# Kernel optimization log

Measured on AMD Instinct MI355X. Metric: run time of the kernel, lower is better.

## Reference

```python
import jax, jax.numpy as jnp
import numpy as np

B, V = 128, 128000
NEG_INF = float('-inf')


def _apply_top_k(logits, top_ks):
    vocab = logits.shape[-1]
    valid_k = jnp.where(top_ks > 0, jnp.minimum(top_ks, vocab), vocab)  # [B]
    order = jnp.argsort(-logits, axis=-1)                 # descending sort indices [B,V]
    sorted_logits = jnp.take_along_axis(logits, order, axis=-1)
    ranks = jnp.arange(vocab)[None, :]                    # [1,V]
    keep = ranks < valid_k[:, None]
    masked_sorted = jnp.where(keep, sorted_logits, NEG_INF)
    rows = jnp.arange(logits.shape[0])[:, None]
    return jnp.zeros_like(logits).at[rows, order].set(masked_sorted)


def _apply_top_p(logits, top_ps):
    order = jnp.argsort(-logits, axis=-1)
    sorted_logits = jnp.take_along_axis(logits, order, axis=-1)
    sorted_probs = jax.nn.softmax(sorted_logits, axis=-1)
    cum = jnp.cumsum(sorted_probs, axis=-1)
    keep = cum < top_ps[:, None]
    keep = keep.at[:, 0].set(True)                        # always keep the top token
    masked_sorted = jnp.where(keep, sorted_logits, NEG_INF)
    rows = jnp.arange(logits.shape[0])[:, None]
    return jnp.zeros_like(logits).at[rows, order].set(masked_sorted)


def setup_inputs() -> dict:
    key = jax.random.key(0)
    k1, k2, k3, k4, k5 = jax.random.split(key, 5)
    logits = jax.random.normal(k1, (B, V), dtype=jnp.float32) * 4.0
    temperatures = jax.random.uniform(k2, (B,), dtype=jnp.float32) + 0.5  # [0.5, 1.5)
    top_ks = jax.random.randint(k3, (B,), 0, 100, dtype=jnp.int64)        # 0 -> disabled
    top_ps = jax.random.uniform(k4, (B,), dtype=jnp.float32)
    # uniform noise; reference converts to Exp(1) via -log(u)
    exp_noise_u = jax.random.uniform(k5, (B, V), dtype=jnp.float32, minval=1e-12, maxval=1.0)
    return {"logits": logits, "temperatures": temperatures, "top_ks": top_ks,
            "top_ps": top_ps, "exp_noise_u": exp_noise_u}


def reference(logits, temperatures, top_ks, top_ps, exp_noise_u):
    x = logits.astype(jnp.float32) / temperatures[:, None]
    x = _apply_top_k(x, top_ks)
    x = _apply_top_p(x, top_ps)
    probs = jax.nn.softmax(x, axis=-1)
    q = jnp.clip(-jnp.log(exp_noise_u), 1e-10)            # Exp(1) samples, clamped like torch
    sample_tokens = jnp.argmax(probs / q, axis=-1)
    return sample_tokens
```

## Files before the change

kernel.cpp:

```cpp
#include <hip/hip_runtime.h>
#include <math.h>

#define SA 8
#define SEG2 8
#define NB 4096
#define TAA 512
#define HS 256
#define TE 512
#define TBB 1024
#define SCT 256
#define CH (NB / SCT)
#define CAPSEG 512
#define GTOT (SA * CAPSEG)
#define MAXM1 16
#define GB1 16384
#define SUBC 512
#define EQC 64
#define FXS 1099511627776.0f
#define FXI (1.0f / 1099511627776.0f)

typedef unsigned u32;
typedef unsigned long long u64;

struct ScanSh {
  u32 axc[SCT]; float axe[SCT];
  u32 sufc[SCT]; float sufe[SCT];
  int cbin[SCT]; u32 cca[SCT]; float cea[SCT];
  int fbin[SCT]; u32 fca[SCT]; float fea[SCT];
};

__device__ __forceinline__ u32 f2key(float f) {
  u32 u = __float_as_uint(f);
  return u ^ ((u >> 31) ? 0xFFFFFFFFu : 0x80000000u);
}
__device__ __forceinline__ int is_mode0(int k, int V) {
  return (k >= 1 && k <= 256 && k < V);
}

__device__ int m1_slot(const int* topks, int row, int V, int tid, int* red) {
  if (tid < 128) {
    int c = 0;
    for (int r = tid; r < row; r += 128) c += !is_mode0(topks[r], V);
    red[tid] = c;
  }
  __syncthreads();
  for (int s = 64; s > 0; s >>= 1) {
    if (tid < s) red[tid] += red[tid + s];
    __syncthreads();
  }
  return red[0];
}

__device__ __forceinline__ float row_max(const float* maxpart, int row) {
  float mm = maxpart[row * SA];
  for (int j = 1; j < SA; ++j) mm = fmaxf(mm, maxpart[row * SA + j]);
  return mm;
}

__device__ void scan_level(const u32* cnt, const u64* e0, ScanSh* ax,
                           u32* sprefix, int* scnt_above, float* sexp_above,
                           float target, int tid) {
  if (tid < SCT) {
    u32 cc = 0; float ce = 0.f; const int base = tid * CH;
    for (int j = 0; j < CH; ++j) { cc += cnt[base + j]; ce += (float)e0[base + j] * FXI; }
    ax->axc[tid] = cc; ax->axe[tid] = ce;
  }
  __syncthreads();
  if (tid == 0) {
    u32 rc = 0; float re = 0.f;
    for (int c = SCT - 1; c >= 0; --c) {
      ax->sufc[c] = rc; ax->sufe[c] = re;
      rc += ax->axc[c]; re += ax->axe[c];
    }
  }
  __syncthreads();
  if (tid < SCT) {
    const int base = tid * CH;
    u32 rc = ax->sufc[tid]; float re = ax->sufe[tid];
    int best = -1; u32 bca = 0; float bea = 0.f;
    int fb = -1; u32 ffca = 0; float ffea = 0.f;
    for (int b = base + CH - 1; b >= base; --b) {
      u32 c = cnt[b]; float ebv = (float)e0[b] * FXI;
      bool cross = (c > 0) && ((re + ebv) >= target);
      if (cross && best < 0) { best = b; bca = rc; bea = re; }
      if (c > 0) { fb = b; ffca = rc; ffea = re; }
      rc += c; re += ebv;
    }
    ax->cbin[tid] = best; ax->cca[tid] = bca; ax->cea[tid] = bea;
    ax->fbin[tid] = fb; ax->fca[tid] = ffca; ax->fea[tid] = ffea;
  }
  __syncthreads();
  if (tid == 0) {
    int bsel = -1; u32 ca = 0; float ea = 0.f;
    for (int c = 0; c < SCT; ++c) {
      int b = ax->cbin[c];
      if (b > bsel) { bsel = b; ca = ax->cca[c]; ea = ax->cea[c]; }
    }
    if (bsel < 0) {
      for (int c = 0; c < SCT; ++c) {
        int b = ax->fbin[c];
        if (b >= 0 && (bsel < 0 || b < bsel)) { bsel = b; ca = ax->fca[c]; ea = ax->fea[c]; }
      }
    }
    if (bsel < 0) bsel = 0;
    *sprefix = (u32)bsel;
    *scnt_above = (int)ca;
    *sexp_above = ea;
  }
  __syncthreads();
}

__global__ __launch_bounds__(TAA) void kA(const float* __restrict__ logits,
                                          const float* __restrict__ temps,
                                          const int* __restrict__ topks,
                                          float* __restrict__ maxpart,
                                          u32* __restrict__ scnt,
                                          float* __restrict__ candv,
                                          int* __restrict__ candi, int V) {
  const int row = blockIdx.x, seg = blockIdx.y, tid = threadIdx.x;
  __shared__ u32 cnt[NB];
  __shared__ float sm[TAA];
  __shared__ u32 cs[HS];
  __shared__ int bb[HS];
  __shared__ int lcnt;
  __shared__ u32 sT;
  const int k = topks[row];
  const int m0 = is_mode0(k, V);
  const float t = temps[row];
  const float* lr = logits + (size_t)row * V;
  const float4* l4 = (const float4*)lr;
  const int n4 = V >> 2;
  const int q0 = (int)((long long)seg * n4 / SA);
  const int q1 = (int)((long long)(seg + 1) * n4 / SA);
  float mx = -INFINITY;
  if (m0) {
    for (int i = tid; i < NB; i += TAA) cnt[i] = 0;
    if (tid == 0) lcnt = 0;
    __syncthreads();
    for (int i = q0 + tid; i < q1; i += TAA) {
      float4 v = l4[i];
      float xs[4] = {v.x / t, v.y / t, v.z / t, v.w / t};
#pragma unroll
      for (int j = 0; j < 4; ++j) {
        mx = fmaxf(mx, xs[j]);
        atomicAdd(&cnt[f2key(xs[j]) >> 20], 1u);
      }
    }
    if (seg == SA - 1)
      for (int i = (n4 << 2) + tid; i < V; i += TAA) {
        float x = lr[i] / t;
        mx = fmaxf(mx, x);
        atomicAdd(&cnt[f2key(x) >> 20], 1u);
      }
  } else {
    for (int i = q0 + tid; i < q1; i += TAA) {
      float4 v = l4[i];
      mx = fmaxf(mx, fmaxf(fmaxf(v.x, v.y), fmaxf(v.z, v.w)) / t);
    }
    if (seg == SA - 1)
      for (int i = (n4 << 2) + tid; i < V; i += TAA) mx = fmaxf(mx, lr[i] / t);
  }
  sm[tid] = mx;
  __syncthreads();
  for (int s = TAA >> 1; s > 0; s >>= 1) {
    if (tid < s) sm[tid] = fmaxf(sm[tid], sm[tid + s]);
    __syncthreads();
  }
  if (tid == 0) maxpart[row * SA + seg] = sm[0];
  if (!m0) return;
  if (tid < HS) {
    u32 cc = 0; const int base = tid * (NB / HS);
    for (int j = 0; j < NB / HS; ++j) cc += cnt[base + j];
    cs[tid] = cc;
  }
  __syncthreads();
  if (tid == 0) {
    u32 rc = 0;
    for (int c = HS - 1; c >= 0; --c) { u32 tmp = cs[c]; cs[c] = rc; rc += tmp; }
  }
  __syncthreads();
  const int kk = (k > 256) ? 256 : k;
  if (tid < HS) {
    const int base = tid * (NB / HS);
    u32 rc = cs[tid]; int best = -1;
    for (int b = base + NB / HS - 1; b >= base; --b) {
      u32 c = cnt[b];
      if (c && best < 0 && (int)(rc + c) >= kk) best = b;
      rc += c;
    }
    bb[tid] = best;
  }
  __syncthreads();
  if (tid == 0) {
    int bsel = -1;
    for (int c = 0; c < HS; ++c) if (bb[c] > bsel) bsel = bb[c];
    if (bsel < 0) { for (int b = 0; b < NB; ++b) if (cnt[b]) { bsel = b; break; } }
    if (bsel < 0) bsel = 0;
    sT = ((u32)bsel) << 20;
  }
  __syncthreads();
  const u32 T = sT;
  const size_t cbase = ((size_t)row * SA + seg) * CAPSEG;
  for (int i = q0 + tid; i < q1; i += TAA) {
    float4 v = l4[i];
    float xs[4] = {v.x / t, v.y / t, v.z / t, v.w / t};
#pragma unroll
    for (int j = 0; j < 4; ++j) {
      if (f2key(xs[j]) >= T) {
        int s = atomicAdd(&lcnt, 1);
        if (s < CAPSEG) { candv[cbase + s] = xs[j]; candi[cbase + s] = i * 4 + j; }
      }
    }
  }
  if (seg == SA - 1)
    for (int i = (n4 << 2) + tid; i < V; i += TAA) {
      float x = lr[i] / t;
      if (f2key(x) >= T) {
        int s = atomicAdd(&lcnt, 1);
        if (s < CAPSEG) { candv[cbase + s] = x; candi[cbase + s] = i; }
      }
    }
  __syncthreads();
  if (tid == 0) { int n = lcnt; if (n > CAPSEG) n = CAPSEG; scnt[row * SA + seg] = (u32)n; }
}

__global__ __launch_bounds__(TE) void kE(const float* __restrict__ logits,
                                         const float* __restrict__ temps,
                                         const int* __restrict__ topks,
                                         const float* __restrict__ maxpart,
                                         float* __restrict__ Sparts,
                                         u32* __restrict__ m1c0,
                                         u64* __restrict__ m1e0, int V) {
  const int row = blockIdx.x, seg = blockIdx.y, tid = threadIdx.x;
  const int k = topks[row];
  if (is_mode0(k, V)) return;
  __shared__ int red[128];
  const int slot = m1_slot(topks, row, V, tid, red);
  if (slot >= MAXM1) return;
  __shared__ u32 c0[NB];
  __shared__ u64 e0[NB];
  __shared__ float ss[TE];
  for (int i = tid; i < NB; i += TE) { c0[i] = 0; e0[i] = 0ull; }
  __syncthreads();
  const float t = temps[row];
  const float m = row_max(maxpart, row);
  const float* lr = logits + (size_t)row * V;
  const float4* l4 = (const float4*)lr;
  const int n4 = V >> 2;
  const int q0 = (int)((long long)seg * n4 / SEG2);
  const int q1 = (int)((long long)(seg + 1) * n4 / SEG2);
  float ls = 0.f;
  for (int i = q0 + tid; i < q1; i += TE) {
    float4 v = l4[i];
    float xs[4] = {v.x / t, v.y / t, v.z / t, v.w / t};
#pragma unroll
    for (int j = 0; j < 4; ++j) {
      float e = expf(xs[j] - m);
      ls += e;
      u32 b = f2key(xs[j]) >> 20;
      atomicAdd(&c0[b], 1u);
      u64 fx = (u64)(e * FXS);
      if (fx) atomicAdd(&e0[b], fx);
    }
  }
  if (seg == SEG2 - 1)
    for (int i = (n4 << 2) + tid; i < V; i += TE) {
      float x = lr[i] / t;
      float e = expf(x - m);
      ls += e;
      u32 b = f2key(x) >> 20;
      atomicAdd(&c0[b], 1u);
      u64 fx = (u64)(e * FXS);
      if (fx) atomicAdd(&e0[b], fx);
    }
  ss[tid] = ls;
  __syncthreads();
  for (int s = TE >> 1; s > 0; s >>= 1) {
    if (tid < s) ss[tid] += ss[tid + s];
    __syncthreads();
  }
  if (tid == 0) Sparts[slot * SEG2 + seg] = ss[0];
  for (int b = tid; b < NB; b += TE) {
    u32 c = c0[b]; if (c) atomicAdd(&m1c0[(size_t)slot * NB + b], c);
    u64 e = e0[b]; if (e) atomicAdd(&m1e0[(size_t)slot * NB + b], e);
  }
}

__global__ __launch_bounds__(TBB) void kM1(const float* __restrict__ logits,
                                           const float* __restrict__ temps,
                                           const int* __restrict__ topks,
                                           const float* __restrict__ topps,
                                           const float* __restrict__ noise,
                                           const float* __restrict__ maxpart,
                                           const float* __restrict__ Sparts,
                                           const u32* __restrict__ m1c0,
                                           const u64* __restrict__ m1e0,
                                           u64* __restrict__ g1p,
                                           u32* __restrict__ gcnt,
                                           u64* __restrict__ rpack,
                                           u32* __restrict__ rdone,
                                           int* __restrict__ out, int V) {
  const int row = blockIdx.x, seg = blockIdx.y, tid = threadIdx.x;
  const int k = topks[row];
  if (is_mode0(k, V)) return;
  __shared__ int red[128];
  const int slot = m1_slot(topks, row, V, tid, red);
  if (slot >= MAXM1) return;

  __shared__ u32 cnt[NB];
  __shared__ u64 e0[NB];
  __shared__ ScanSh ax;
  __shared__ u32 spfx; __shared__ int sca; __shared__ float sea;
  __shared__ float rr[TBB]; __shared__ int ri[TBB];
  for (int i = tid; i < NB; i += TBB) {
    cnt[i] = m1c0[(size_t)slot * NB + i];
    e0[i] = m1e0[(size_t)slot * NB + i];
  }
  __syncthreads();
  float S = 0.f;
  for (int j = 0; j < SEG2; ++j) S += Sparts[slot * SEG2 + j];
  const float target = topps[row] * S;
  scan_level(cnt, e0, &ax, &spfx, &sca, &sea, target, tid);
  const u32 pfx = spfx;

  const float t = temps[row];
  const float m = row_max(maxpart, row);
  const float* lr = logits + (size_t)row * V;
  const float* ur = noise + (size_t)row * V;
  const float4* l4 = (const float4*)lr;
  const float4* u4 = (const float4*)ur;
  const int n4 = V >> 2;
  const int q0 = (int)((long long)seg * n4 / SEG2);
  const int q1 = (int)((long long)(seg + 1) * n4 / SEG2);
  const size_t gbase = (size_t)slot * GB1;

  float best = -1.f; int bidx = 0x7FFFFFFF;
  for (int i = q0 + tid; i < q1; i += TBB) {
    float4 xv = l4[i];
    float4 uv = u4[i];
    float xs[4] = {xv.x / t, xv.y / t, xv.z / t, xv.w / t};
    float us[4] = {uv.x, uv.y, uv.z, uv.w};
#pragma unroll
    for (int j = 0; j < 4; ++j) {
      u32 key = f2key(xs[j]);
      u32 bin = key >> 20;
      int idx = i * 4 + j;
      if (bin == pfx) {
        u32 s2 = atomicAdd(&gcnt[slot], 1u);
        if (s2 < GB1)
          atomicExch(&g1p[gbase + s2],
                     ((u64)__float_as_uint(xs[j]) << 32) | (u64)(u32)idx);
      } else if (bin > pfx) {
        float q = fmaxf(-logf(us[j]), 1e-10f);
        float rt = expf(xs[j] - m) / q;
        if (rt > best || (rt == best && idx < bidx)) { best = rt; bidx = idx; }
      }
    }
  }
  if (seg == SEG2 - 1)
    for (int i = (n4 << 2) + tid; i < V; i += TBB) {
      float x = lr[i] / t;
      u32 key = f2key(x);
      u32 bin = key >> 20;
      if (bin == pfx) {
        u32 s2 = atomicAdd(&gcnt[slot], 1u);
        if (s2 < GB1)
          atomicExch(&g1p[gbase + s2],
                     ((u64)__float_as_uint(x) << 32) | (u64)(u32)i);
      } else if (bin > pfx) {
        float q = fmaxf(-logf(ur[i]), 1e-10f);
        float rt = expf(x - m) / q;
        if (rt > best || (rt == best && i < bidx)) { best = rt; bidx = i; }
      }
    }
  rr[tid] = best; ri[tid] = bidx;
  __syncthreads();
  for (int s = TBB >> 1; s > 0; s >>= 1) {
    if (tid < s) {
      float ov = rr[tid + s]; int oi = ri[tid + s];
      if (ov > rr[tid] || (ov == rr[tid] && oi < ri[tid])) { rr[tid] = ov; ri[tid] = oi; }
    }
    __syncthreads();
  }
  __shared__ int slast;
  if (tid == 0) {
    if (rr[0] >= 0.f) {
      u64 pk = ((u64)f2key(rr[0]) << 32) | (u64)(0xFFFFFFFFu - (u32)ri[0]);
      atomicMax(&rpack[row], pk);
    }
    __threadfence();
    u32 arr = atomicAdd(&rdone[row], 1u);
    slast = (arr == (u32)(SEG2 - 1)) ? 1 : 0;
  }
  __syncthreads();
  if (!slast) return;
  __threadfence();

  __shared__ u32 cnt1[1024]; __shared__ u64 fx1[1024];
  __shared__ u32 csuf[1024]; __shared__ u64 esuf[1024];
  __shared__ float subv[SUBC]; __shared__ int subi[SUBC];
  __shared__ float ssv[SUBC]; __shared__ int ssi[SUBC];
  __shared__ int eqs[EQC];
  __shared__ int scross, sfb, sca1, sns, seqn;
  __shared__ float sea1; __shared__ u32 svstar;

  int nf = (int)atomicAdd(&gcnt[slot], 0u);
  if (nf > GB1) nf = GB1;
  cnt1[tid] = 0; fx1[tid] = 0ull;
  if (tid == 0) { sns = 0; scross = -1; sfb = 0x7FFFFFFF; }
  __syncthreads();
  for (int i = tid; i < nf; i += TBB) {
    u64 p = atomicAdd(&g1p[gbase + i], 0ull);
    float x = __uint_as_float((u32)(p >> 32));
    u32 b = (f2key(x) >> 10) & 0x3FFu;
    float e = expf(x - m);
    atomicAdd(&cnt1[b], 1u);
    u64 fx = (u64)(e * FXS);
    if (fx) atomicAdd(&fx1[b], fx);
  }
  __syncthreads();
  csuf[tid] = cnt1[tid]; esuf[tid] = fx1[tid];
  __syncthreads();
  for (int stp = 1; stp < 1024; stp <<= 1) {
    u32 ca_ = 0; u64 ea_ = 0ull;
    if (tid + stp < 1024) { ca_ = csuf[tid + stp]; ea_ = esuf[tid + stp]; }
    __syncthreads();
    csuf[tid] += ca_; esuf[tid] += ea_;
    __syncthreads();
  }
  {
    u32 c = cnt1[tid];
    if (c) {
      float racc = (float)(esuf[tid] - fx1[tid]) * FXI;
      float ebv = (float)fx1[tid] * FXI;
      if (sea + (racc + ebv) >= target) atomicMax(&scross, tid);
      atomicMin(&sfb, tid);
    }
  }
  __syncthreads();
  if (tid == 0) {
    int cb = scross;
    if (cb < 0) cb = (sfb != 0x7FFFFFFF) ? sfb : 0;
    u32 cAbove = csuf[cb] - cnt1[cb];
    float eAbove = (float)(esuf[cb] - fx1[cb]) * FXI;
    scross = cb;
    sea1 = sea + eAbove;
    sca1 = sca + (int)cAbove;
  }
  __syncthreads();
  const u32 cb = (u32)scross;
  for (int i = tid; i < nf; i += TBB) {
    u64 p = atomicAdd(&g1p[gbase + i], 0ull);
    float x = __uint_as_float((u32)(p >> 32));
    if (((f2key(x) >> 10) & 0x3FFu) == cb) {
      int s2 = atomicAdd(&sns, 1);
      if (s2 < SUBC) { subv[s2] = x; subi[s2] = (int)(u32)(p & 0xFFFFFFFFull); }
    }
  }
  __syncthreads();
  int ns = sns; if (ns > SUBC) ns = SUBC;
  for (int i = tid; i < ns; i += TBB) {
    float v = subv[i]; int ix = subi[i];
    int rank = 0;
    for (int j2 = 0; j2 < ns; ++j2) {
      float vj = subv[j2]; int ij = subi[j2];
      if (vj > v || (vj == v && ij < ix)) rank++;
    }
    ssv[rank] = v; ssi[rank] = ix;
  }
  __syncthreads();
  if (tid == 0) {
    const float p = topps[row];
    float run_n = sea1 / S;
    const int have_above = (sca1 > 0);
    u32 lastkey = 0u; int lastr = 0, laststart = -1, anykept = 0;
    u32 vsel = 0u; int rsel = -1, bstart = 0;
    int j = 0;
    while (j < ns) {
      u32 key = f2key(ssv[j]);
      int c = 1;
      while (j + c < ns && f2key(ssv[j + c]) == key) ++c;
      float e = expf(ssv[j] - m);
      float en = e / S;
      int kept = 0;
      for (int q = 0; q < c; ++q) {
        float nn = run_n + en;
        if (nn < p) { run_n = nn; kept++; } else break;
      }
      if (kept == c) { lastkey = key; lastr = c; laststart = j; anykept = 1; j += c; continue; }
      if (kept > 0) { vsel = key; rsel = kept; bstart = j; }
      else if (anykept) { vsel = lastkey; rsel = lastr; bstart = laststart; }
      else if (have_above) { vsel = key; rsel = 0; bstart = j; }
      else { vsel = key; rsel = 1; bstart = j; }
      break;
    }
    if (rsel < 0) {
      if (anykept) { vsel = lastkey; rsel = lastr; bstart = laststart; }
      else if (ns > 0) {
        vsel = f2key(ssv[0]); bstart = 0;
        rsel = have_above ? 0 : 1;
      } else { vsel = 0u; rsel = 0; bstart = 0; }
    }
    int eqn = rsel;
    if (eqn > EQC) eqn = EQC;
    if (eqn < 0) eqn = 0;
    if (bstart + eqn > ns) eqn = ns - bstart;
    if (eqn < 0) eqn = 0;
    for (int q2 = 0; q2 < eqn; ++q2) eqs[q2] = ssi[bstart + q2];
    seqn = eqn; svstar = vsel;
  }
  __syncthreads();

  const u32 vk = svstar;
  const int eqn = seqn;
  best = -1.f; bidx = 0x7FFFFFFF;
  for (int i = tid; i < nf; i += TBB) {
    u64 p = atomicAdd(&g1p[gbase + i], 0ull);
    float x = __uint_as_float((u32)(p >> 32));
    int ix = (int)(u32)(p & 0xFFFFFFFFull);
    u32 key = f2key(x);
    bool kept = key > vk;
    if (!kept && key == vk) {
      for (int e = 0; e < eqn; ++e) if (eqs[e] == ix) { kept = true; break; }
    }
    if (kept) {
      float q = fmaxf(-logf(ur[ix]), 1e-10f);
      float rt = expf(x - m) / q;
      if (rt > best || (rt == best && ix < bidx)) { best = rt; bidx = ix; }
    }
  }
  rr[tid] = best; ri[tid] = bidx;
  __syncthreads();
  for (int s = TBB >> 1; s > 0; s >>= 1) {
    if (tid < s) {
      float ov = rr[tid + s]; int oi = ri[tid + s];
      if (ov > rr[tid] || (ov == rr[tid] && oi < ri[tid])) { rr[tid] = ov; ri[tid] = oi; }
    }
    __syncthreads();
  }
  if (tid == 0) {
    u64 myPk = 0ull;
    if (rr[0] >= 0.f)
      myPk = ((u64)f2key(rr[0]) << 32) | (u64)(0xFFFFFFFFu - (u32)ri[0]);
    u64 prev = atomicMax(&rpack[row], myPk);
    u64 fin = prev > myPk ? prev : myPk;
    out[row] = (int)(0xFFFFFFFFu - (u32)(fin & 0xFFFFFFFFull));
  }
}

__global__ __launch_bounds__(TBB) void kH(const float* __restrict__ topps,
                                          const float* __restrict__ noise,
                                          const int* __restrict__ topks,
                                          const float* __restrict__ maxpart,
                                          const u32* __restrict__ scnt,
                                          const float* __restrict__ candv,
                                          const int* __restrict__ candi,
                                          int* __restrict__ out, int V) {
  const int row = blockIdx.x, tid = threadIdx.x;
  const int kR = topks[row];
  if (!is_mode0(kR, V)) return;
  __shared__ float gv[GTOT]; __shared__ int gi[GTOT];
  __shared__ float sv[CAPSEG]; __shared__ int si[CAPSEG];
  __shared__ float fv[CAPSEG]; __shared__ int fi[CAPSEG];
  __shared__ float pe[CAPSEG];
  __shared__ float rr[TBB]; __shared__ int ri[TBB];
  __shared__ int offs[SA + 1];
  __shared__ u32 dh[256]; __shared__ u32 dsufx[256];
  __shared__ u32 sPrefix; __shared__ int sRemain, sNf, sDig;
  __shared__ int sJ; __shared__ float sZ2;
  if (tid == 0) {
    int o = 0;
    for (int s = 0; s < SA; ++s) {
      offs[s] = o;
      int c = (int)scnt[row * SA + s];
      if (c > CAPSEG) c = CAPSEG;
      if (c < 0) c = 0;
      o += c;
    }
    offs[SA] = o;
  }
  __syncthreads();
  const int g = offs[SA];
  for (int s = 0; s < SA; ++s) {
    const int o = offs[s], c = offs[s + 1] - o;
    const size_t cbase = ((size_t)row * SA + s) * CAPSEG;
    for (int i = tid; i < c; i += TBB) { gv[o + i] = candv[cbase + i]; gi[o + i] = candi[cbase + i]; }
  }
  __syncthreads();
  int kk = kR; if (kk > 256) kk = 256; if (kk > g) kk = g;
  if (tid == 0) { sPrefix = 0u; sRemain = (kk < 1) ? 1 : kk; }
  __syncthreads();
  for (int pass = 0; pass < 4; ++pass) {
    const int shift = 24 - 8 * pass;
    if (tid < 256) dh[tid] = 0;
    if (tid == 0) sDig = -1;
    __syncthreads();
    const u32 pref = sPrefix;
    for (int i = tid; i < g; i += TBB) {
      u32 key = f2key(gv[i]);
      if (pass == 0 || (key >> (shift + 8)) == pref)
        atomicAdd(&dh[(key >> shift) & 0xFFu], 1u);
    }
    __syncthreads();
    if (tid < 256) dsufx[tid] = dh[tid];
    __syncthreads();
    for (int stp = 1; stp < 256; stp <<= 1) {
      u32 addv = 0;
      if (tid < 256 && tid + stp < 256) addv = dsufx[tid + stp];
      __syncthreads();
      if (tid < 256) dsufx[tid] += addv;
      __syncthreads();
    }
    if (tid < 256) {
      u32 excl = dsufx[tid] - dh[tid];
      u32 rem = (u32)sRemain;
      if (dh[tid] && excl < rem && excl + dh[tid] >= rem) sDig = tid;
    }
    __syncthreads();
    if (tid == 0) {
      int d = sDig; if (d < 0) d = 0;
      u32 excl = dsufx[d] - dh[d];
      sRemain -= (int)excl;
      sPrefix = (sPrefix << 8) | (u32)d;
      if (pass == 3) sNf = 0;
    }
    __syncthreads();
  }
  const u32 Tk = sPrefix;
  for (int i = tid; i < g; i += TBB) {
    if (f2key(gv[i]) >= Tk) {
      int s = atomicAdd(&sNf, 1);
      if (s < CAPSEG) { fv[s] = gv[i]; fi[s] = gi[i]; }
    }
  }
  __syncthreads();
  int nf = sNf; if (nf > CAPSEG) nf = CAPSEG;
  for (int i = tid; i < nf; i += TBB) {
    float v = fv[i]; int ix = fi[i];
    int rank = 0;
    for (int j = 0; j < nf; ++j) {
      float vj = fv[j]; int ij = fi[j];
      if (vj > v || (vj == v && ij < ix)) rank++;
    }
    sv[rank] = v; si[rank] = ix;
  }
  __syncthreads();
  const float m = row_max(maxpart, row);
  const float p = topps[row];
  int keff = kR; if (keff > nf) keff = nf;
  for (int j = tid; j < keff; j += TBB) pe[j] = expf(sv[j] - m);
  __syncthreads();
  if (tid == 0) {
    int J = 1; float Z2 = 1.f;
    if (nf > 0 && keff > 0) {
      float Zk = 0.f;
      for (int j = 0; j < keff; ++j) Zk += pe[j];
      float c = 0.f; int Jc = 0;
      for (int j = 0; j < keff; ++j) {
        float pr = pe[j] / Zk;
        c += pr;
        if (c < p) Jc++;
      }
      if (Jc < 1) Jc = 1;
      J = Jc;
      Z2 = 0.f;
      for (int j = 0; j < J && j < keff; ++j) Z2 += pe[j];
    }
    sJ = J; sZ2 = Z2;
  }
  __syncthreads();
  const int J = sJ; const float Z2 = sZ2;
  float best = -1.f; int bidx = 0x7FFFFFFF;
  for (int j = tid; j < J && j < nf; j += TBB) {
    int ix = si[j];
    float u = noise[(size_t)row * V + ix];
    float q = fmaxf(-logf(u), 1e-10f);
    float pr = pe[j] / Z2;
    float rt = pr / q;
    if (rt > best || (rt == best && ix < bidx)) { best = rt; bidx = ix; }
  }
  rr[tid] = best; ri[tid] = bidx;
  __syncthreads();
  for (int s = TBB >> 1; s > 0; s >>= 1) {
    if (tid < s) {
      float ov = rr[tid + s]; int oi = ri[tid + s];
      if (ov > rr[tid] || (ov == rr[tid] && oi < ri[tid])) { rr[tid] = ov; ri[tid] = oi; }
    }
    __syncthreads();
  }
  if (tid == 0) out[row] = (nf > 0) ? ri[0] : 0;
}

extern "C" void kernel_launch(void* const* d_in, const int* in_sizes, int n_in,
                              void* d_out, int out_size, void* d_ws, size_t ws_size,
                              hipStream_t stream) {
  const float* logits = (const float*)d_in[0];
  const float* temps = (const float*)d_in[1];
  const int* topks = (const int*)d_in[2];
  const float* topps = (const float*)d_in[3];
  const float* noise = (const float*)d_in[4];
  int* out = (int*)d_out;
  const int B = in_sizes[1];
  const int V = in_sizes[0] / B;
  (void)n_in; (void)out_size; (void)ws_size;

  u32* w = (u32*)d_ws;
  size_t o = 0;
  float* maxpart = (float*)(w + o); o += (size_t)B * SA;
  u32* scnt = w + o; o += (size_t)B * SA;
  float* candv = (float*)(w + o); o += (size_t)B * SA * CAPSEG;
  int* candi = (int*)(w + o); o += (size_t)B * SA * CAPSEG;
  if (o & 1) o += 1;
  const size_t zbase = o;
  u64* m1e0 = (u64*)(w + o); o += 2 * (size_t)MAXM1 * NB;
  u32* m1c0 = w + o; o += (size_t)MAXM1 * NB;
  u64* rpack = (u64*)(w + o); o += 2 * (size_t)B;
  u32* rdone = w + o; o += (size_t)B;
  u32* gcnt = w + o; o += MAXM1;
  if (o & 1) o += 1;
  const size_t zwords = o - zbase;
  float* Sparts = (float*)(w + o); o += (size_t)MAXM1 * SEG2;
  if (o & 1) o += 1;
  u64* g1p = (u64*)(w + o); o += 2 * (size_t)MAXM1 * GB1;

  hipMemsetAsync((void*)(w + zbase), 0, zwords * sizeof(u32), stream);
  kA<<<dim3(B, SA), TAA, 0, stream>>>(logits, temps, topks, maxpart, scnt, candv, candi, V);
  kE<<<dim3(B, SEG2), TE, 0, stream>>>(logits, temps, topks, maxpart, Sparts, m1c0, m1e0, V);
  kM1<<<dim3(B, SEG2), TBB, 0, stream>>>(logits, temps, topks, topps, noise, maxpart,
                                         Sparts, m1c0, m1e0, g1p, gcnt, rpack, rdone, out, V);
  kH<<<B, TBB, 0, stream>>>(topps, noise, topks, maxpart, scnt, candv, candi, out, V);
}
```

Measured before the change: 239.7 us.

## Fuse histogram and candidate passes into one kernel with per-bin winners

Merges the histogram/exp-sum kernel and the top-p filtering kernel into a single kernel. In one pass it builds per-bin counts, exp sums and per-bin best sampling scores, then scatters every element bucket-sorted into a workspace so a last-arriving block can do the threshold scan and refine only the boundary bin. The separate memset is also folded into kA. This saves one kernel launch and a second pass over logits and noise, at the cost of a full-vocabulary scatter per segment, heavier shared-memory use and many more atomics.

```diff
diff --git a/kernel.cpp b/kernel.cpp
--- a/kernel.cpp
+++ b/kernel.cpp
@@ -6,14 +6,12 @@
 #define NB 4096
 #define TAA 512
 #define HS 256
-#define TE 512
 #define TBB 1024
 #define SCT 256
 #define CH (NB / SCT)
 #define CAPSEG 512
 #define GTOT (SA * CAPSEG)
 #define MAXM1 16
-#define GB1 16384
 #define SUBC 512
 #define EQC 64
 #define FXS 1099511627776.0f
@@ -116,7 +114,9 @@
                                           float* __restrict__ maxpart,
                                           u32* __restrict__ scnt,
                                           float* __restrict__ candv,
-                                          int* __restrict__ candi, int V) {
+                                          int* __restrict__ candi,
+                                          u32* __restrict__ zp, size_t zwords,
+                                          int V) {
   const int row = blockIdx.x, seg = blockIdx.y, tid = threadIdx.x;
   __shared__ u32 cnt[NB];
   __shared__ float sm[TAA];
@@ -124,6 +124,11 @@
   __shared__ int bb[HS];
   __shared__ int lcnt;
   __shared__ u32 sT;
+  {
+    const size_t gid = ((size_t)blockIdx.y * gridDim.x + blockIdx.x) * TAA + tid;
+    const size_t stride = (size_t)gridDim.x * gridDim.y * TAA;
+    for (size_t i = gid; i < zwords; i += stride) zp[i] = 0;
+  }
   const int k = topks[row];
   const int m0 = is_mode0(k, V);
   const float t = temps[row];
@@ -224,104 +229,45 @@
   if (tid == 0) { int n = lcnt; if (n > CAPSEG) n = CAPSEG; scnt[row * SA + seg] = (u32)n; }
 }
 
-__global__ __launch_bounds__(TE) void kE(const float* __restrict__ logits,
-                                         const float* __restrict__ temps,
-                                         const int* __restrict__ topks,
-                                         const float* __restrict__ maxpart,
-                                         float* __restrict__ Sparts,
-                                         u32* __restrict__ m1c0,
-                                         u64* __restrict__ m1e0, int V) {
+__global__ __launch_bounds__(TBB) void kM(const float* __restrict__ logits,
+                                          const float* __restrict__ temps,
+                                          const int* __restrict__ topks,
+                                          const float* __restrict__ topps,
+                                          const float* __restrict__ noise,
+                                          const float* __restrict__ maxpart,
+                                          float* __restrict__ Sparts,
+                                          u32* __restrict__ m1c0,
+                                          u64* __restrict__ m1e0,
+                                          u64* __restrict__ m1w,
+                                          u32* __restrict__ m1sb,
+                                          u64* __restrict__ g1all,
+                                          u32* __restrict__ rdoneM,
+                                          int* __restrict__ out, int V) {
   const int row = blockIdx.x, seg = blockIdx.y, tid = threadIdx.x;
   const int k = topks[row];
   if (is_mode0(k, V)) return;
   __shared__ int red[128];
   const int slot = m1_slot(topks, row, V, tid, red);
   if (slot >= MAXM1) return;
-  __shared__ u32 c0[NB];
-  __shared__ u64 e0[NB];
-  __shared__ float ss[TE];
-  for (int i = tid; i < NB; i += TE) { c0[i] = 0; e0[i] = 0ull; }
-  __syncthreads();
-  const float t = temps[row];
-  const float m = row_max(maxpart, row);
-  const float* lr = logits + (size_t)row * V;
-  const float4* l4 = (const float4*)lr;
-  const int n4 = V >> 2;
-  const int q0 = (int)((long long)seg * n4 / SEG2);
-  const int q1 = (int)((long long)(seg + 1) * n4 / SEG2);
-  float ls = 0.f;
-  for (int i = q0 + tid; i < q1; i += TE) {
-    float4 v = l4[i];
-    float xs[4] = {v.x / t, v.y / t, v.z / t, v.w / t};
-#pragma unroll
-    for (int j = 0; j < 4; ++j) {
-      float e = expf(xs[j] - m);
-      ls += e;
-      u32 b = f2key(xs[j]) >> 20;
-      atomicAdd(&c0[b], 1u);
-      u64 fx = (u64)(e * FXS);
-      if (fx) atomicAdd(&e0[b], fx);
-    }
-  }
-  if (seg == SEG2 - 1)
-    for (int i = (n4 << 2) + tid; i < V; i += TE) {
-      float x = lr[i] / t;
-      float e = expf(x - m);
-      ls += e;
-      u32 b = f2key(x) >> 20;
-      atomicAdd(&c0[b], 1u);
-      u64 fx = (u64)(e * FXS);
-      if (fx) atomicAdd(&e0[b], fx);
-    }
-  ss[tid] = ls;
-  __syncthreads();
-  for (int s = TE >> 1; s > 0; s >>= 1) {
-    if (tid < s) ss[tid] += ss[tid + s];
-    __syncthreads();
-  }
-  if (tid == 0) Sparts[slot * SEG2 + seg] = ss[0];
-  for (int b = tid; b < NB; b += TE) {
-    u32 c = c0[b]; if (c) atomicAdd(&m1c0[(size_t)slot * NB + b], c);
-    u64 e = e0[b]; if (e) atomicAdd(&m1e0[(size_t)slot * NB + b], e);
-  }
-}
-
-__global__ __launch_bounds__(TBB) void kM1(const float* __restrict__ logits,
-                                           const float* __restrict__ temps,
-                                           const int* __restrict__ topks,
-                                           const float* __restrict__ topps,
-                                           const float* __restrict__ noise,
-                                           const float* __restrict__ maxpart,
-                                           const float* __restrict__ Sparts,
-                                           const u32* __restrict__ m1c0,
-                                           const u64* __restrict__ m1e0,
-                                           u64* __restrict__ g1p,
-                                           u32* __restrict__ gcnt,
-                                           u64* __restrict__ rpack,
-                                           u32* __restrict__ rdone,
-                                           int* __restrict__ out, int V) {
-  const int row = blockIdx.x, seg = blockIdx.y, tid = threadIdx.x;
-  const int k = topks[row];
-  if (is_mode0(k, V)) return;
-  __shared__ int red[128];
-  const int slot = m1_slot(topks, row, V, tid, red);
-  if (slot >= MAXM1) return;
 
   __shared__ u32 cnt[NB];
   __shared__ u64 e0[NB];
+  __shared__ u64 wtab[NB];
+  __shared__ float ss[TBB];
+  __shared__ u32 psc[TBB];
   __shared__ ScanSh ax;
+  __shared__ u32 cnt1[1024]; __shared__ u64 fx1[1024];
+  __shared__ u32 csuf[1024]; __shared__ u64 esuf[1024];
+  __shared__ float subv[SUBC]; __shared__ int subi[SUBC];
+  __shared__ float ssv[SUBC]; __shared__ int ssi[SUBC];
+  __shared__ u64 rrp[TBB];
+  __shared__ int eqs[EQC];
+  __shared__ int segoff[SEG2]; __shared__ int segn[SEG2]; __shared__ int segcum[SEG2 + 1];
   __shared__ u32 spfx; __shared__ int sca; __shared__ float sea;
-  __shared__ float rr[TBB]; __shared__ int ri[TBB];
-  for (int i = tid; i < NB; i += TBB) {
-    cnt[i] = m1c0[(size_t)slot * NB + i];
-    e0[i] = m1e0[(size_t)slot * NB + i];
-  }
-  __syncthreads();
-  float S = 0.f;
-  for (int j = 0; j < SEG2; ++j) S += Sparts[slot * SEG2 + j];
-  const float target = topps[row] * S;
-  scan_level(cnt, e0, &ax, &spfx, &sca, &sea, target, tid);
-  const u32 pfx = spfx;
+  __shared__ float sS;
+  __shared__ int scross, sfb, sca1, sns, seqn;
+  __shared__ float sea1; __shared__ u32 svstar;
+  __shared__ int slast;
 
   const float t = temps[row];
   const float m = row_max(maxpart, row);
@@ -332,85 +278,159 @@
   const int n4 = V >> 2;
   const int q0 = (int)((long long)seg * n4 / SEG2);
   const int q1 = (int)((long long)(seg + 1) * n4 / SEG2);
-  const size_t gbase = (size_t)slot * GB1;
-
-  float best = -1.f; int bidx = 0x7FFFFFFF;
+  const int eb0 = q0 << 2;
+
+  for (int i = tid; i < NB; i += TBB) { cnt[i] = 0; e0[i] = 0ull; wtab[i] = 0ull; }
+  __syncthreads();
+
+  float ls = 0.f;
   for (int i = q0 + tid; i < q1; i += TBB) {
-    float4 xv = l4[i];
-    float4 uv = u4[i];
+    float4 xv = l4[i]; float4 uv = u4[i];
     float xs[4] = {xv.x / t, xv.y / t, xv.z / t, xv.w / t};
     float us[4] = {uv.x, uv.y, uv.z, uv.w};
 #pragma unroll
     for (int j = 0; j < 4; ++j) {
-      u32 key = f2key(xs[j]);
-      u32 bin = key >> 20;
-      int idx = i * 4 + j;
-      if (bin == pfx) {
-        u32 s2 = atomicAdd(&gcnt[slot], 1u);
-        if (s2 < GB1)
-          atomicExch(&g1p[gbase + s2],
-                     ((u64)__float_as_uint(xs[j]) << 32) | (u64)(u32)idx);
-      } else if (bin > pfx) {
-        float q = fmaxf(-logf(us[j]), 1e-10f);
-        float rt = expf(xs[j] - m) / q;
-        if (rt > best || (rt == best && idx < bidx)) { best = rt; bidx = idx; }
-      }
+      float e = expf(xs[j] - m);
+      ls += e;
+      u32 b = f2key(xs[j]) >> 20;
+      atomicAdd(&cnt[b], 1u);
+      u64 fx = (u64)(e * FXS);
+      if (fx) atomicAdd(&e0[b], fx);
+      float q = fmaxf(-logf(us[j]), 1e-10f);
+      float rt = e / q;
+      u64 wp = ((u64)f2key(rt) << 32) | (u64)(0xFFFFFFFFu - (u32)(i * 4 + j));
+      atomicMax(&wtab[b], wp);
     }
   }
   if (seg == SEG2 - 1)
     for (int i = (n4 << 2) + tid; i < V; i += TBB) {
       float x = lr[i] / t;
-      u32 key = f2key(x);
-      u32 bin = key >> 20;
-      if (bin == pfx) {
-        u32 s2 = atomicAdd(&gcnt[slot], 1u);
-        if (s2 < GB1)
-          atomicExch(&g1p[gbase + s2],
-                     ((u64)__float_as_uint(x) << 32) | (u64)(u32)i);
-      } else if (bin > pfx) {
-        float q = fmaxf(-logf(ur[i]), 1e-10f);
-        float rt = expf(x - m) / q;
-        if (rt > best || (rt == best && i < bidx)) { best = rt; bidx = i; }
-      }
-    }
-  rr[tid] = best; ri[tid] = bidx;
+      float e = expf(x - m);
+      ls += e;
+      u32 b = f2key(x) >> 20;
+      atomicAdd(&cnt[b], 1u);
+      u64 fx = (u64)(e * FXS);
+      if (fx) atomicAdd(&e0[b], fx);
+      float q = fmaxf(-logf(ur[i]), 1e-10f);
+      float rt = e / q;
+      u64 wp = ((u64)f2key(rt) << 32) | (u64)(0xFFFFFFFFu - (u32)i);
+      atomicMax(&wtab[b], wp);
+    }
+  ss[tid] = ls;
   __syncthreads();
   for (int s = TBB >> 1; s > 0; s >>= 1) {
-    if (tid < s) {
-      float ov = rr[tid + s]; int oi = ri[tid + s];
-      if (ov > rr[tid] || (ov == rr[tid] && oi < ri[tid])) { rr[tid] = ov; ri[tid] = oi; }
-    }
-    __syncthreads();
-  }
-  __shared__ int slast;
-  if (tid == 0) {
-    if (rr[0] >= 0.f) {
-      u64 pk = ((u64)f2key(rr[0]) << 32) | (u64)(0xFFFFFFFFu - (u32)ri[0]);
-      atomicMax(&rpack[row], pk);
-    }
+    if (tid < s) ss[tid] += ss[tid + s];
+    __syncthreads();
+  }
+  if (tid == 0)
+    atomicExch((u32*)&Sparts[slot * SEG2 + seg], __float_as_uint(ss[0]));
+
+  for (int b = tid; b < NB; b += TBB) {
+    u32 c = cnt[b]; if (c) atomicAdd(&m1c0[(size_t)slot * NB + b], c);
+    u64 e = e0[b]; if (e) atomicAdd(&m1e0[(size_t)slot * NB + b], e);
+    u64 w = wtab[b]; if (w) atomicMax(&m1w[(size_t)slot * NB + b], w);
+  }
+
+  u32 c4[4]; u32 tsum = 0;
+#pragma unroll
+  for (int j = 0; j < 4; ++j) { c4[j] = cnt[tid * 4 + j]; tsum += c4[j]; }
+  psc[tid] = tsum;
+  __syncthreads();
+  for (int stp = 1; stp < TBB; stp <<= 1) {
+    u32 v = 0;
+    if (tid >= stp) v = psc[tid - stp];
+    __syncthreads();
+    psc[tid] += v;
+    __syncthreads();
+  }
+  u32* lbase = (u32*)wtab;
+  {
+    u32 run = psc[tid] - tsum;
+    const size_t sbb = ((size_t)slot * SEG2 + seg) * (size_t)(NB + 1);
+#pragma unroll
+    for (int j = 0; j < 4; ++j) {
+      lbase[tid * 4 + j] = run;
+      atomicExch(&m1sb[sbb + (size_t)(tid * 4 + j)], run);
+      run += c4[j];
+    }
+    if (tid == 0) atomicExch(&m1sb[sbb + NB], psc[TBB - 1]);
+  }
+  __syncthreads();
+  for (int i = tid; i < NB; i += TBB) cnt[i] = 0;
+  __syncthreads();
+
+  const size_t gseg = (size_t)slot * V + (size_t)eb0;
+  for (int i = q0 + tid; i < q1; i += TBB) {
+    float4 xv = l4[i];
+    float xs[4] = {xv.x / t, xv.y / t, xv.z / t, xv.w / t};
+#pragma unroll
+    for (int j = 0; j < 4; ++j) {
+      u32 b = f2key(xs[j]) >> 20;
+      u32 r = atomicAdd(&cnt[b], 1u);
+      atomicExch(&g1all[gseg + (size_t)(lbase[b] + r)],
+                 ((u64)__float_as_uint(xs[j]) << 32) | (u64)(u32)(i * 4 + j));
+    }
+  }
+  if (seg == SEG2 - 1)
+    for (int i = (n4 << 2) + tid; i < V; i += TBB) {
+      float x = lr[i] / t;
+      u32 b = f2key(x) >> 20;
+      u32 r = atomicAdd(&cnt[b], 1u);
+      atomicExch(&g1all[gseg + (size_t)(lbase[b] + r)],
+                 ((u64)__float_as_uint(x) << 32) | (u64)(u32)i);
+    }
+  __syncthreads();
+
+  if (tid == 0) {
     __threadfence();
-    u32 arr = atomicAdd(&rdone[row], 1u);
+    u32 arr = atomicAdd(&rdoneM[row], 1u);
     slast = (arr == (u32)(SEG2 - 1)) ? 1 : 0;
   }
   __syncthreads();
   if (!slast) return;
   __threadfence();
 
-  __shared__ u32 cnt1[1024]; __shared__ u64 fx1[1024];
-  __shared__ u32 csuf[1024]; __shared__ u64 esuf[1024];
-  __shared__ float subv[SUBC]; __shared__ int subi[SUBC];
-  __shared__ float ssv[SUBC]; __shared__ int ssi[SUBC];
-  __shared__ int eqs[EQC];
-  __shared__ int scross, sfb, sca1, sns, seqn;
-  __shared__ float sea1; __shared__ u32 svstar;
-
-  int nf = (int)atomicAdd(&gcnt[slot], 0u);
-  if (nf > GB1) nf = GB1;
+  for (int i = tid; i < NB; i += TBB) {
+    cnt[i] = atomicAdd(&m1c0[(size_t)slot * NB + i], 0u);
+    e0[i] = atomicAdd(&m1e0[(size_t)slot * NB + i], 0ull);
+  }
+  if (tid == 0) {
+    float S = 0.f;
+    for (int j = 0; j < SEG2; ++j)
+      S += __uint_as_float(atomicAdd((u32*)&Sparts[slot * SEG2 + j], 0u));
+    sS = S;
+    sns = 0; scross = -1; sfb = 0x7FFFFFFF;
+  }
+  __syncthreads();
+  const float S = sS;
+  const float target = topps[row] * S;
+  scan_level(cnt, e0, &ax, &spfx, &sca, &sea, target, tid);
+  const u32 pfx = spfx;
+
+  if (tid < SEG2) {
+    const int qq0 = (int)((long long)tid * n4 / SEG2);
+    const size_t sbb = ((size_t)slot * SEG2 + tid) * (size_t)(NB + 1);
+    int st0 = (int)atomicAdd(&m1sb[sbb + pfx], 0u);
+    int st1 = (int)atomicAdd(&m1sb[sbb + pfx + 1], 0u);
+    segoff[tid] = (qq0 << 2) + st0;
+    segn[tid] = st1 - st0;
+  }
+  __syncthreads();
+  if (tid == 0) {
+    int c = 0;
+    for (int s = 0; s < SEG2; ++s) { segcum[s] = c; c += segn[s]; }
+    segcum[SEG2] = c;
+  }
+  __syncthreads();
+  const int nf = segcum[SEG2];
+  const size_t gslot = (size_t)slot * V;
+
   cnt1[tid] = 0; fx1[tid] = 0ull;
-  if (tid == 0) { sns = 0; scross = -1; sfb = 0x7FFFFFFF; }
   __syncthreads();
   for (int i = tid; i < nf; i += TBB) {
-    u64 p = atomicAdd(&g1p[gbase + i], 0ull);
+    int s = 0;
+    while (i >= segcum[s + 1]) ++s;
+    u64 p = atomicAdd(&g1all[gslot + (size_t)(segoff[s] + (i - segcum[s]))], 0ull);
     float x = __uint_as_float((u32)(p >> 32));
     u32 b = (f2key(x) >> 10) & 0x3FFu;
     float e = expf(x - m);
@@ -450,7 +470,9 @@
   __syncthreads();
   const u32 cb = (u32)scross;
   for (int i = tid; i < nf; i += TBB) {
-    u64 p = atomicAdd(&g1p[gbase + i], 0ull);
+    int s = 0;
+    while (i >= segcum[s + 1]) ++s;
+    u64 p = atomicAdd(&g1all[gslot + (size_t)(segoff[s] + (i - segcum[s]))], 0ull);
     float x = __uint_as_float((u32)(p >> 32));
     if (((f2key(x) >> 10) & 0x3FFu) == cb) {
       int s2 = atomicAdd(&sns, 1);
@@ -511,11 +533,17 @@
   }
   __syncthreads();
 
+  u64 best = 0ull;
+  for (int b = (int)pfx + 1 + tid; b < NB; b += TBB) {
+    u64 w = atomicAdd(&m1w[(size_t)slot * NB + b], 0ull);
+    if (w > best) best = w;
+  }
   const u32 vk = svstar;
   const int eqn = seqn;
-  best = -1.f; bidx = 0x7FFFFFFF;
   for (int i = tid; i < nf; i += TBB) {
-    u64 p = atomicAdd(&g1p[gbase + i], 0ull);
+    int s = 0;
+    while (i >= segcum[s + 1]) ++s;
+    u64 p = atomicAdd(&g1all[gslot + (size_t)(segoff[s] + (i - segcum[s]))], 0ull);
     float x = __uint_as_float((u32)(p >> 32));
     int ix = (int)(u32)(p & 0xFFFFFFFFull);
     u32 key = f2key(x);
@@ -526,26 +554,18 @@
     if (kept) {
       float q = fmaxf(-logf(ur[ix]), 1e-10f);
       float rt = expf(x - m) / q;
-      if (rt > best || (rt == best && ix < bidx)) { best = rt; bidx = ix; }
-    }
-  }
-  rr[tid] = best; ri[tid] = bidx;
+      u64 wp = ((u64)f2key(rt) << 32) | (u64)(0xFFFFFFFFu - (u32)ix);
+      if (wp > best) best = wp;
+    }
+  }
+  rrp[tid] = best;
   __syncthreads();
   for (int s = TBB >> 1; s > 0; s >>= 1) {
-    if (tid < s) {
-      float ov = rr[tid + s]; int oi = ri[tid + s];
-      if (ov > rr[tid] || (ov == rr[tid] && oi < ri[tid])) { rr[tid] = ov; ri[tid] = oi; }
-    }
-    __syncthreads();
-  }
-  if (tid == 0) {
-    u64 myPk = 0ull;
-    if (rr[0] >= 0.f)
-      myPk = ((u64)f2key(rr[0]) << 32) | (u64)(0xFFFFFFFFu - (u32)ri[0]);
-    u64 prev = atomicMax(&rpack[row], myPk);
-    u64 fin = prev > myPk ? prev : myPk;
-    out[row] = (int)(0xFFFFFFFFu - (u32)(fin & 0xFFFFFFFFull));
-  }
+    if (tid < s) { if (rrp[tid + s] > rrp[tid]) rrp[tid] = rrp[tid + s]; }
+    __syncthreads();
+  }
+  if (tid == 0)
+    out[row] = (rrp[0] != 0ull) ? (int)(0xFFFFFFFFu - (u32)(rrp[0] & 0xFFFFFFFFull)) : 0;
 }
 
 __global__ __launch_bounds__(TBB) void kH(const float* __restrict__ topps,
@@ -712,21 +732,20 @@
   int* candi = (int*)(w + o); o += (size_t)B * SA * CAPSEG;
   if (o & 1) o += 1;
   const size_t zbase = o;
+  u32* m1c0 = w + o; o += (size_t)MAXM1 * NB;
   u64* m1e0 = (u64*)(w + o); o += 2 * (size_t)MAXM1 * NB;
-  u32* m1c0 = w + o; o += (size_t)MAXM1 * NB;
-  u64* rpack = (u64*)(w + o); o += 2 * (size_t)B;
-  u32* rdone = w + o; o += (size_t)B;
-  u32* gcnt = w + o; o += MAXM1;
-  if (o & 1) o += 1;
+  u64* m1w = (u64*)(w + o); o += 2 * (size_t)MAXM1 * NB;
+  u32* rdoneM = w + o; o += (size_t)B;
   const size_t zwords = o - zbase;
   float* Sparts = (float*)(w + o); o += (size_t)MAXM1 * SEG2;
+  u32* m1sb = w + o; o += (size_t)MAXM1 * SEG2 * (NB + 1);
   if (o & 1) o += 1;
-  u64* g1p = (u64*)(w + o); o += 2 * (size_t)MAXM1 * GB1;
-
-  hipMemsetAsync((void*)(w + zbase), 0, zwords * sizeof(u32), stream);
-  kA<<<dim3(B, SA), TAA, 0, stream>>>(logits, temps, topks, maxpart, scnt, candv, candi, V);
-  kE<<<dim3(B, SEG2), TE, 0, stream>>>(logits, temps, topks, maxpart, Sparts, m1c0, m1e0, V);
-  kM1<<<dim3(B, SEG2), TBB, 0, stream>>>(logits, temps, topks, topps, noise, maxpart,
-                                         Sparts, m1c0, m1e0, g1p, gcnt, rpack, rdone, out, V);
+  u64* g1all = (u64*)(w + o); o += 2 * (size_t)MAXM1 * V;
+
+  kA<<<dim3(B, SA), TAA, 0, stream>>>(logits, temps, topks, maxpart, scnt,
+                                      candv, candi, w + zbase, zwords, V);
+  kM<<<dim3(B, SEG2), TBB, 0, stream>>>(logits, temps, topks, topps, noise, maxpart,
+                                        Sparts, m1c0, m1e0, m1w, m1sb, g1all,
+                                        rdoneM, out, V);
   kH<<<B, TBB, 0, stream>>>(topps, noise, topks, maxpart, scnt, candv, candi, out, V);
 }
```

Result: slower. 260.8 us (+8.8%).
